# Performance work log

Measured on AMD Instinct MI355X. Metric: run time of the kernel, lower is better.

## Reference

```python
import jax, jax.numpy as jnp
import numpy as np

N = 50000      # nodes
E = 800000     # edges (avg degree 16)
F_IN = 128
HID = 64
NCLS = 40
K = 2          # num_stacks
T = 2          # num_layers (shared weights)


def setup_inputs() -> dict:
    key = jax.random.key(0)
    ks = jax.random.split(key, 10)
    s = 0.05
    return {
        "x": jax.random.normal(ks[0], (N, F_IN), dtype=jnp.float32),
        "edge_index": jax.random.randint(ks[1], (2, E), 0, N),
        "w1_init": jax.random.normal(ks[2], (K, F_IN, HID), dtype=jnp.float32) * s,
        "w1": jax.random.normal(ks[3], (K, HID, HID), dtype=jnp.float32) * s,
        "v1": jax.random.normal(ks[4], (K, F_IN, HID), dtype=jnp.float32) * s,
        "b1": jax.random.normal(ks[5], (K, HID), dtype=jnp.float32) * s,
        "w2_init": jax.random.normal(ks[6], (K, HID, NCLS), dtype=jnp.float32) * s,
        "w2": jax.random.normal(ks[7], (K, NCLS, NCLS), dtype=jnp.float32) * s,
        "v2": jax.random.normal(ks[8], (K, HID, NCLS), dtype=jnp.float32) * s,
        "b2": jax.random.normal(ks[9], (K, NCLS), dtype=jnp.float32) * s,
    }


def _gcn_norm(src, dst, n):
    # PyG gcn_norm with add_self_loops=False: deg over destination, sym norm
    deg = jax.ops.segment_sum(jnp.ones_like(dst, dtype=jnp.float32), dst, num_segments=n)
    dinv = jnp.where(deg > 0, 1.0 / jnp.sqrt(deg), 0.0)
    return dinv[src] * dinv[dst]  # [E]


def _arma_conv(x, src, dst, norm, n, w_init, w, v, b, act):
    # x: [N, Fin]; w_init: [K, Fin, Fout]; w: [K, Fout, Fout]; v: [K, Fin, Fout]; b: [K, Fout]
    root = jnp.einsum('nf,kfg->kng', x, v)  # [K, N, Fout], dropout=0 -> identity
    out = None
    for t in range(T):
        if t == 0:
            h = jnp.einsum('nf,kfg->kng', x, w_init)
        else:
            h = jnp.einsum('knf,kfg->kng', out, w)
        # sparse neighbor aggregation: out[i] = sum_{(j->i)} norm_e * h[j]
        agg = jax.vmap(
            lambda hk: jax.ops.segment_sum(hk[src] * norm[:, None], dst, num_segments=n)
        )(h)  # [K, N, Fout]
        out = act(agg + root + b[:, None, :])
    return out.mean(axis=0)  # mean over stacks -> [N, Fout]


def reference(x, edge_index, w1_init, w1, v1, b1, w2_init, w2, v2, b2):
    src, dst = edge_index[0], edge_index[1]
    norm = _gcn_norm(src, dst, N)
    h = _arma_conv(x, src, dst, norm, N, w1_init, w1, v1, b1, jax.nn.relu)
    h = jax.nn.relu(h)  # wrapper ReLU; dropout is identity in eval
    o = _arma_conv(h, src, dst, norm, N, w2_init, w2, v2, b2, lambda z: z)
    return jax.nn.log_softmax(o, axis=1)
```

## Files before the change

### kernel.cpp

```cpp
#include <hip/hip_runtime.h>
#include <hip/hip_bf16.h>
#include <math.h>

#define N_NODES 50000
#define F_IN 128
#define HID 64
#define NCLS 40
#define K_STACKS 2
#define SCAN_TILE 1024
#define NBLK_CNT 256

typedef __attribute__((ext_vector_type(8))) short short8;
typedef __attribute__((ext_vector_type(4))) float floatx4;
typedef __attribute__((ext_vector_type(2))) float floatx2;

__device__ __forceinline__ unsigned int f32_to_bf16_bits(float f) {
    unsigned int u = __float_as_uint(f);
    return (u + 0x7fffu + ((u >> 16) & 1u)) >> 16;
}
__device__ __forceinline__ unsigned int pack_bf16x2(float a, float b) {
    return f32_to_bf16_bits(a) | (f32_to_bf16_bits(b) << 16);
}
__device__ __forceinline__ unsigned char f32_to_fp8(float v) {
    int pk = __builtin_amdgcn_cvt_pk_fp8_f32(v, v, 0, false);
    return (unsigned char)(pk & 0xff);
}


__global__ __launch_bounds__(256) void count_kernel(const int* __restrict__ dst,
                                                    int* __restrict__ counts,
                                                    int* __restrict__ tileSums, int E) {
    __shared__ int hist[256];
    __shared__ int ts[64];
    int blk = blockIdx.x, t = threadIdx.x;
    hist[t] = 0;
    if (t < 64) ts[t] = 0;
    __syncthreads();
    int chunk = (E + NBLK_CNT - 1) / NBLK_CNT;
    int s = blk * chunk, e = min(E, s + chunk);
    for (int i = s + t; i < e; i += 256) atomicAdd(&hist[dst[i] >> 8], 1);
    __syncthreads();
    counts[t * NBLK_CNT + blk] = hist[t];
    atomicAdd(&ts[t >> 2], hist[t]);
    __syncthreads();
    if (t < 64) atomicAdd(&tileSums[t], ts[t]);
}

__global__ __launch_bounds__(256) void scan_phase3_excl(const int* __restrict__ in,
                                                        const int* __restrict__ tileSums,
                                                        int* __restrict__ out, int n) {
    __shared__ int lds[256];
    __shared__ int tsum[64];
    int b = blockIdx.x, t = threadIdx.x;
    if (t < 64) tsum[t] = tileSums[t];
    int base = b * SCAN_TILE + t * 4;
    int e[4];
    int s = 0;
#pragma unroll
    for (int i = 0; i < 4; ++i) {
        e[i] = (base + i < n) ? in[base + i] : 0;
        s += e[i];
    }
    lds[t] = s;
    __syncthreads();
    int v = s;
    for (int off = 1; off < 256; off <<= 1) {
        int add = (t >= off) ? lds[t - off] : 0;
        __syncthreads();
        v += add;
        lds[t] = v;
        __syncthreads();
    }
    int toff = 0;
    for (int i = 0; i < b; ++i) toff += tsum[i];
    int run = (t == 0 ? 0 : lds[t - 1]) + toff;
#pragma unroll
    for (int i = 0; i < 4; ++i) {
        if (base + i < n) {
            out[base + i] = run;
            run += e[i];
        }
    }
}

__global__ __launch_bounds__(256) void bucket_scatter_kernel(const int* __restrict__ src,
                                                             const int* __restrict__ dst,
                                                             const int* __restrict__ scanned,
                                                             unsigned int* __restrict__ pairs,
                                                             int E) {
    __shared__ int cur[256];
    int blk = blockIdx.x, t = threadIdx.x;
    cur[t] = scanned[t * NBLK_CNT + blk];
    __syncthreads();
    int chunk = (E + NBLK_CNT - 1) / NBLK_CNT;
    int s0 = blk * chunk, e0 = min(E, s0 + chunk);
    for (int i = s0 + t; i < e0; i += 256) {
        int d = dst[i];
        int pos = atomicAdd(&cur[d >> 8], 1);
        pairs[pos] = (unsigned int)src[i] | ((unsigned int)(d & 255) << 16);
    }
}

__global__ __launch_bounds__(256) void csr_build_kernel(const unsigned int* __restrict__ pairs,
                                                        const int* __restrict__ scanned,
                                                        int* __restrict__ row_ptr,
                                                        float* __restrict__ dinv,
                                                        int* __restrict__ col, int N, int E) {
    __shared__ int degl[256], lds[256], curl[256], sb[2];
    int b = blockIdx.x, t = threadIdx.x;
    if (t == 0) {
        sb[0] = scanned[b * NBLK_CNT];
        sb[1] = (b + 1 < 256) ? scanned[(b + 1) * NBLK_CNT] : E;
    }
    degl[t] = 0;
    __syncthreads();
    int bstart = sb[0], bend = sb[1];
    for (int e = bstart + t; e < bend; e += 256) {
        atomicAdd(&degl[(pairs[e] >> 16) & 255], 1);
    }
    __syncthreads();
    int d = degl[t];
    lds[t] = d;
    __syncthreads();
    int v = d;
    for (int off = 1; off < 256; off <<= 1) {
        int add = (t >= off) ? lds[t - off] : 0;
        __syncthreads();
        v += add;
        lds[t] = v;
        __syncthreads();
    }
    int excl = v - d;
    int node = b * 256 + t;
    if (node <= N) row_ptr[node] = bstart + excl;
    if (node < N) dinv[node] = (d > 0) ? (1.0f / sqrtf((float)d)) : 0.0f;
    curl[t] = excl;
    __syncthreads();
    for (int e = bstart + t; e < bend; e += 256) {
        unsigned int p = pairs[e];
        int ln = (p >> 16) & 255;
        int pos = atomicAdd(&curl[ln], 1);
        col[bstart + pos] = (int)(p & 0xffffu);
    }
}

__device__ __forceinline__ void wt_one(const float* __restrict__ in,
                                       unsigned short* __restrict__ out, int li, int C, int F,
                                       int CP) {
    int k = li / (F * CP);
    int r = li - k * F * CP;
    int f = r / CP;
    int c = r - f * CP;
    out[li] = (c < C) ? (unsigned short)f32_to_bf16_bits(in[((size_t)k * C + c) * F + f]) : 0;
}

__global__ void wt_all_kernel(const float* v1, const float* w1i, const float* w1,
                              const float* v2, const float* w2i, const float* w2,
                              unsigned short* v1t, unsigned short* w1it, unsigned short* w1t,
                              unsigned short* v2t, unsigned short* w2it, unsigned short* w2t) {
    int i = blockIdx.x * blockDim.x + threadIdx.x;
    if (i < 16384) wt_one(v1, v1t, i, 128, 64, 128);
    else if (i < 32768) wt_one(w1i, w1it, i - 16384, 128, 64, 128);
    else if (i < 40960) wt_one(w1, w1t, i - 32768, 64, 64, 64);
    else if (i < 46080) wt_one(v2, v2t, i - 40960, 64, 40, 64);
    else if (i < 51200) wt_one(w2i, w2it, i - 46080, 64, 40, 64);
    else if (i < 56320) wt_one(w2, w2t, i - 51200, 40, 40, 64);
}

template <int CINP>
__device__ __forceinline__ void stage_A(const void* A, unsigned short* At, size_t abase,
                                        int n0, int t, int N, int CREAL, int a_bf16) {
    constexpr int CP8 = CINP / 8;
    constexpr int MS = CP8 - 1;
    constexpr int SH = (CP8 == 16) ? 4 : 3;
    for (int i = t; i < 64 * CP8; i += 256) {
        int n = i >> SH;
        int c = i & MS;
        uint4 w = make_uint4(0u, 0u, 0u, 0u);
        int gn = n0 + n;
        if (gn < N && c * 8 < CREAL) {
            if (a_bf16) {
                w = *(const uint4*)((const unsigned short*)A + abase + (size_t)gn * CREAL + c * 8);
            } else {
                const float* srcp = (const float*)A + abase + (size_t)gn * CREAL + c * 8;
                float4 f0 = *(const float4*)(srcp);
                float4 f1 = *(const float4*)(srcp + 4);
                w.x = pack_bf16x2(f0.x, f0.y);
                w.y = pack_bf16x2(f0.z, f0.w);
                w.z = pack_bf16x2(f1.x, f1.y);
                w.w = pack_bf16x2(f1.z, f1.w);
            }
        }
        *(uint4*)(At + n * CINP + ((c ^ (n & MS)) << 3)) = w;
    }
}

template <int CINP>
__device__ __forceinline__ void stage_B(const unsigned short* Bk, unsigned short* Bs, int t,
                                        int COUT) {
    constexpr int CP8 = CINP / 8;
    constexpr int MS = CP8 - 1;
    constexpr int SH = (CP8 == 16) ? 4 : 3;
    for (int i = t; i < COUT * CP8; i += 256) {
        int f = i >> SH;
        int c = i & MS;
        uint4 w = *(const uint4*)(Bk + f * CINP + c * 8);
        *(uint4*)(Bs + f * CINP + ((c ^ (f & MS)) << 3)) = w;
    }
}

__global__ __launch_bounds__(256) void gemm12_kernel(
    const float* __restrict__ A, const unsigned short* __restrict__ Bt1,
    const unsigned short* __restrict__ Bt2, unsigned short* __restrict__ out1,
    unsigned char* __restrict__ out2, const float* __restrict__ scale, int N) {
    constexpr int CINP = 128;
    constexpr int MS = 15;
    __shared__ __align__(16) unsigned short At[64 * CINP];
    __shared__ __align__(16) unsigned short Bs1[64 * CINP];
    __shared__ __align__(16) unsigned short Bs2[64 * CINP];
    const int n0 = blockIdx.x * 64;
    const int t = threadIdx.x;
    stage_A<CINP>(A, At, 0, n0, t, N, CINP, 0);
    const int lane = t & 63;
    const int wv = t >> 6;
    const int quad = lane >> 4;
    const int li = lane & 15;
    const int m0 = wv * 16;
    const int am = (m0 + li) & MS;
#pragma unroll 1
    for (int k = 0; k < 2; ++k) {
        stage_B<CINP>(Bt1 + (size_t)k * 64 * CINP, Bs1, t, 64);
        stage_B<CINP>(Bt2 + (size_t)k * 64 * CINP, Bs2, t, 64);
        __syncthreads();
        floatx4 acc1[4] = {{0.f, 0.f, 0.f, 0.f}, {0.f, 0.f, 0.f, 0.f},
                           {0.f, 0.f, 0.f, 0.f}, {0.f, 0.f, 0.f, 0.f}};
        floatx4 acc2[4] = {{0.f, 0.f, 0.f, 0.f}, {0.f, 0.f, 0.f, 0.f},
                           {0.f, 0.f, 0.f, 0.f}, {0.f, 0.f, 0.f, 0.f}};
#pragma unroll
        for (int kc = 0; kc < 4; ++kc) {
            int cc = kc * 4 + quad;
            short8 a = *(const short8*)(At + (m0 + li) * CINP + ((cc ^ am) << 3));
#pragma unroll
            for (int nt = 0; nt < 4; ++nt) {
                int f = nt * 16 + li;
                int bo = f * CINP + ((cc ^ (f & MS)) << 3);
                short8 b1 = *(const short8*)(Bs1 + bo);
                short8 b2 = *(const short8*)(Bs2 + bo);
                acc1[nt] = __builtin_amdgcn_mfma_f32_16x16x32_bf16(a, b1, acc1[nt], 0, 0, 0);
                acc2[nt] = __builtin_amdgcn_mfma_f32_16x16x32_bf16(a, b2, acc2[nt], 0, 0, 0);
            }
        }
        float sc[4];
#pragma unroll
        for (int r = 0; r < 4; ++r) {
            int node = n0 + m0 + quad * 4 + r;
            sc[r] = (node < N) ? scale[node] : 1.f;
        }
#pragma unroll
        for (int nt = 0; nt < 4; ++nt) {
            int f = nt * 16 + li;
#pragma unroll
            for (int r = 0; r < 4; ++r) {
                int node = n0 + m0 + quad * 4 + r;
                if (node < N) {
                    out1[((size_t)k * N + node) * 64 + f] =
                        (unsigned short)f32_to_bf16_bits(acc1[nt][r]);
                    out2[(size_t)node * 128 + (size_t)k * 64 + f] = f32_to_fp8(acc2[nt][r] * sc[r]);
                }
            }
        }
        __syncthreads();
    }
}

template <int F, int COUT, int FMODE>
__global__ __launch_bounds__(256) void agg_gemm_kernel(
    const unsigned char* __restrict__ h8, const int* __restrict__ row_ptr,
    const int* __restrict__ col, const float* __restrict__ dinv,
    const unsigned short* __restrict__ rootb, const float* __restrict__ bias,
    const unsigned short* __restrict__ Bt1, const unsigned short* __restrict__ Bt2,
    unsigned short* __restrict__ rootOut, unsigned char* __restrict__ tblOut, int N) {
    constexpr int NA = (FMODE == 1) ? 1 : 2;
    constexpr int NB = (FMODE == 1) ? 4 : 2;
    constexpr int BT = COUT * 64;
    constexpr int NT = (COUT + 15) / 16;
    constexpr int FH = F / 8;
    constexpr int ROWB = 2 * F;
    __shared__ __align__(16) unsigned short At[NA * 64 * 64];
    __shared__ __align__(16) unsigned short Bs[NB * BT];
    __shared__ int rp[65];
    __shared__ float dvl[64];

    const int n0 = blockIdx.x * 64;
    const int t = threadIdx.x;

    stage_B<64>(Bt1, Bs, t, COUT);
    stage_B<64>(Bt1 + (size_t)COUT * 64, Bs + BT, t, COUT);
    if constexpr (FMODE == 1) {
        stage_B<64>(Bt2, Bs + 2 * BT, t, COUT);
        stage_B<64>(Bt2 + (size_t)COUT * 64, Bs + 3 * BT, t, COUT);
    }
    if (t < 65) rp[t] = row_ptr[min(n0 + t, N)];
    if (t < 64) dvl[t] = (n0 + t < N) ? dinv[n0 + t] : 0.f;
    __syncthreads();

    const int lane = t & 63;
    const int wv = t >> 6;
    const int half = lane >> 5;
    const int l32 = lane & 31;
    const int sub = l32 >> 4;
    const int fq = l32 & 15;
    const int kk = fq >> 3;
    const int fqq = fq & 7;
    const int fqc = (fqq < FH) ? fqq : (FH - 1);
    const int foff = kk * F + fqc * 8;

#pragma unroll 1
    for (int p = 0; p < 8; ++p) {
        const int nl = wv * 16 + p * 2 + half;
        const int node = n0 + nl;
        const bool valid = node < N;
        const int e0 = rp[nl];
        const int deg = rp[nl + 1] - e0;
        const float dv = dvl[nl];
        float acc[8] = {};
        for (int w0 = 0; w0 < deg; w0 += 32) {
            int mye = w0 + l32;
            int c = (mye < deg) ? col[e0 + mye] : 0;
            int nch = min(deg - w0, 32);
            for (int base = 0; base < nch; base += 16) {
                uint2 v[8];
                float wj[8];
#pragma unroll
                for (int u = 0; u < 8; ++u) {
                    int j = base + u * 2 + sub;
                    int cj = __shfl(c, (half << 5) | (j & 31));
                    bool ok = (j < nch);
                    wj[u] = ok ? 1.f : 0.f;
                    int cs = ok ? cj : 0;
                    v[u] = *(const uint2*)(h8 + (size_t)cs * ROWB + foff);
                }
#pragma unroll
                for (int u = 0; u < 8; ++u) {
                    floatx2 f0 = __builtin_amdgcn_cvt_pk_f32_fp8(v[u].x, false);
                    floatx2 f1 = __builtin_amdgcn_cvt_pk_f32_fp8(v[u].x, true);
                    floatx2 f2 = __builtin_amdgcn_cvt_pk_f32_fp8(v[u].y, false);
                    floatx2 f3 = __builtin_amdgcn_cvt_pk_f32_fp8(v[u].y, true);
                    acc[0] += wj[u] * f0.x;
                    acc[1] += wj[u] * f0.y;
                    acc[2] += wj[u] * f1.x;
                    acc[3] += wj[u] * f1.y;
                    acc[4] += wj[u] * f2.x;
                    acc[5] += wj[u] * f2.y;
                    acc[6] += wj[u] * f3.x;
                    acc[7] += wj[u] * f3.y;
                }
            }
        }
#pragma unroll
        for (int i = 0; i < 8; ++i) acc[i] += __shfl_xor(acc[i], 16);

        size_t oc = ((size_t)kk * N + (valid ? node : 0)) * F + fqc * 8;
        uint4 rv = *(const uint4*)(rootb + oc);
        const float* bp = bias + kk * F + fqc * 8;
        float4 b0 = *(const float4*)(bp);
        float4 b1_ = *(const float4*)(bp + 4);
        const unsigned int ru[4] = {rv.x, rv.y, rv.z, rv.w};
        float res[8];
#pragma unroll
        for (int q = 0; q < 4; ++q) {
            float rlo = __uint_as_float(ru[q] << 16);
            float rhi = __uint_as_float(ru[q] & 0xffff0000u);
            float blo = (q < 2) ? ((q == 0) ? b0.x : b0.z) : ((q == 2) ? b1_.x : b1_.z);
            float bhi = (q < 2) ? ((q == 0) ? b0.y : b0.w) : ((q == 2) ? b1_.y : b1_.w);
            res[2 * q] = acc[2 * q] * dv + rlo + blo;
            res[2 * q + 1] = acc[2 * q + 1] * dv + rhi + bhi;
        }
        if constexpr (FMODE != 2) {
#pragma unroll
            for (int i = 0; i < 8; ++i) res[i] = fmaxf(res[i], 0.f);
        }
        if constexpr (FMODE == 1) {
            float mres[8];
#pragma unroll
            for (int i = 0; i < 8; ++i) mres[i] = 0.5f * (res[i] + __shfl_xor(res[i], 8));
            if (sub == 0 && kk == 0) {
                uint4 w;
                w.x = pack_bf16x2(mres[0], mres[1]);
                w.y = pack_bf16x2(mres[2], mres[3]);
                w.z = pack_bf16x2(mres[4], mres[5]);
                w.w = pack_bf16x2(mres[6], mres[7]);
                *(uint4*)(At + nl * 64 + ((fqq ^ (nl & 7)) << 3)) = w;
            }
        } else {
            if (sub == 0) {
                uint4 w = make_uint4(0u, 0u, 0u, 0u);
                if (fqq < FH) {
                    w.x = pack_bf16x2(res[0], res[1]);
                    w.y = pack_bf16x2(res[2], res[3]);
                    w.z = pack_bf16x2(res[4], res[5]);
                    w.w = pack_bf16x2(res[6], res[7]);
                }
                *(uint4*)(At + kk * 4096 + nl * 64 + ((fqq ^ (nl & 7)) << 3)) = w;
            }
        }
    }
    __syncthreads();

    const int quad = lane >> 4;
    const int li = lane & 15;
    const int m0 = wv * 16;
    const int am = (m0 + li) & 7;

    if constexpr (FMODE == 1) {
        floatx4 aR[2][NT] = {};
        floatx4 aT[2][NT] = {};
#pragma unroll
        for (int kc = 0; kc < 2; ++kc) {
            int cc = kc * 4 + quad;
            short8 a = *(const short8*)(At + (m0 + li) * 64 + ((cc ^ am) << 3));
#pragma unroll
            for (int nt = 0; nt < NT; ++nt) {
                int f = nt * 16 + li;
                int fc = (COUT & 15) ? ((f < COUT) ? f : (COUT - 1)) : f;
                int bo = fc * 64 + ((cc ^ (fc & 7)) << 3);
#pragma unroll
                for (int k = 0; k < 2; ++k) {
                    short8 bR = *(const short8*)(Bs + k * BT + bo);
                    short8 bT = *(const short8*)(Bs + (2 + k) * BT + bo);
                    aR[k][nt] = __builtin_amdgcn_mfma_f32_16x16x32_bf16(a, bR, aR[k][nt], 0, 0, 0);
                    aT[k][nt] = __builtin_amdgcn_mfma_f32_16x16x32_bf16(a, bT, aT[k][nt], 0, 0, 0);
                }
            }
        }
#pragma unroll
        for (int k = 0; k < 2; ++k) {
#pragma unroll
            for (int nt = 0; nt < NT; ++nt) {
                int f = nt * 16 + li;
                if (f >= COUT) continue;
#pragma unroll
                for (int r = 0; r < 4; ++r) {
                    int nl2 = m0 + quad * 4 + r;
                    int node = n0 + nl2;
                    if (node < N) {
                        rootOut[((size_t)k * N + node) * COUT + f] =
                            (unsigned short)f32_to_bf16_bits(aR[k][nt][r]);
                        tblOut[(size_t)node * 2 * COUT + (size_t)k * COUT + f] =
                            f32_to_fp8(aT[k][nt][r] * dvl[nl2]);
                    }
                }
            }
        }
    } else {
        floatx4 ac[2][NT] = {};
#pragma unroll
        for (int kc = 0; kc < 2; ++kc) {
            int cc = kc * 4 + quad;
            int ao = (m0 + li) * 64 + ((cc ^ am) << 3);
            short8 a0 = *(const short8*)(At + ao);
            short8 a1 = *(const short8*)(At + 4096 + ao);
#pragma unroll
            for (int nt = 0; nt < NT; ++nt) {
                int f = nt * 16 + li;
                int fc = (COUT & 15) ? ((f < COUT) ? f : (COUT - 1)) : f;
                int bo = fc * 64 + ((cc ^ (fc & 7)) << 3);
                short8 b0 = *(const short8*)(Bs + bo);
                short8 b1v = *(const short8*)(Bs + BT + bo);
                ac[0][nt] = __builtin_amdgcn_mfma_f32_16x16x32_bf16(a0, b0, ac[0][nt], 0, 0, 0);
                ac[1][nt] = __builtin_amdgcn_mfma_f32_16x16x32_bf16(a1, b1v, ac[1][nt], 0, 0, 0);
            }
        }
#pragma unroll
        for (int k = 0; k < 2; ++k) {
#pragma unroll
            for (int nt = 0; nt < NT; ++nt) {
                int f = nt * 16 + li;
                if (f >= COUT) continue;
#pragma unroll
                for (int r = 0; r < 4; ++r) {
                    int nl2 = m0 + quad * 4 + r;
                    int node = n0 + nl2;
                    if (node < N)
                        tblOut[(size_t)node * 2 * COUT + (size_t)k * COUT + f] =
                            f32_to_fp8(ac[k][nt][r] * dvl[nl2]);
                }
            }
        }
    }
}

template <int F>
__global__ __launch_bounds__(256) void agg_kernel(
    const unsigned char* __restrict__ h8, const int* __restrict__ row_ptr,
    const int* __restrict__ col, const float* __restrict__ dinv,
    const unsigned short* __restrict__ rootb, const float* __restrict__ bias,
    void* __restrict__ out, int N, int do_relu, int mode) {
    constexpr int FH = F / 8;
    constexpr int ROWB = 2 * F;
    int wid = (blockIdx.x * blockDim.x + threadIdx.x) >> 6;
    int lane = threadIdx.x & 63;
    int half = lane >> 5;
    int l32 = lane & 31;
    int node = wid * 2 + half;
    bool valid = node < N;
    int e0 = 0, deg = 0;
    float dv = 0.f;
    if (valid) {
        e0 = row_ptr[node];
        deg = row_ptr[node + 1] - e0;
        dv = dinv[node];
    }
    const int sub = l32 >> 4;
    const int fq = l32 & 15;
    const int kk = fq >> 3;
    const int fqq = fq & 7;
    const int fqc = (fqq < FH) ? fqq : (FH - 1);
    const int foff = kk * F + fqc * 8;

    float acc[8] = {};
    for (int w0 = 0; w0 < deg; w0 += 32) {
        int mye = w0 + l32;
        int c = (mye < deg) ? col[e0 + mye] : 0;
        int nch = min(deg - w0, 32);
        for (int base = 0; base < nch; base += 16) {
            uint2 v[8];
            float wj[8];
#pragma unroll
            for (int u = 0; u < 8; ++u) {
                int j = base + u * 2 + sub;
                int cj = __shfl(c, (half << 5) | (j & 31));
                bool ok = (j < nch);
                wj[u] = ok ? 1.f : 0.f;
                int cs = ok ? cj : 0;
                v[u] = *(const uint2*)(h8 + (size_t)cs * ROWB + foff);
            }
#pragma unroll
            for (int u = 0; u < 8; ++u) {
                floatx2 f0 = __builtin_amdgcn_cvt_pk_f32_fp8(v[u].x, false);
                floatx2 f1 = __builtin_amdgcn_cvt_pk_f32_fp8(v[u].x, true);
                floatx2 f2 = __builtin_amdgcn_cvt_pk_f32_fp8(v[u].y, false);
                floatx2 f3 = __builtin_amdgcn_cvt_pk_f32_fp8(v[u].y, true);
                acc[0] += wj[u] * f0.x;
                acc[1] += wj[u] * f0.y;
                acc[2] += wj[u] * f1.x;
                acc[3] += wj[u] * f1.y;
                acc[4] += wj[u] * f2.x;
                acc[5] += wj[u] * f2.y;
                acc[6] += wj[u] * f3.x;
                acc[7] += wj[u] * f3.y;
            }
        }
    }
#pragma unroll
    for (int i = 0; i < 8; ++i) acc[i] += __shfl_xor(acc[i], 16);

    size_t oc = ((size_t)kk * N + (valid ? node : 0)) * F + fqc * 8;
    uint4 rv = *(const uint4*)(rootb + oc);
    const float* bp = bias + kk * F + fqc * 8;
    float4 b0 = *(const float4*)(bp);
    float4 b1 = *(const float4*)(bp + 4);
    const unsigned int ru[4] = {rv.x, rv.y, rv.z, rv.w};
    float res[8];
#pragma unroll
    for (int q = 0; q < 4; ++q) {
        float rlo = __uint_as_float(ru[q] << 16);
        float rhi = __uint_as_float(ru[q] & 0xffff0000u);
        float blo = (q < 2) ? ((q == 0) ? b0.x : b0.z) : ((q == 2) ? b1.x : b1.z);
        float bhi = (q < 2) ? ((q == 0) ? b0.y : b0.w) : ((q == 2) ? b1.y : b1.w);
        res[2 * q] = acc[2 * q] * dv + rlo + blo;
        res[2 * q + 1] = acc[2 * q + 1] * dv + rhi + bhi;
    }
    if (do_relu) {
#pragma unroll
        for (int i = 0; i < 8; ++i) res[i] = fmaxf(res[i], 0.f);
    }
    if (mode == 0) {
        if (sub == 0 && fqq < FH && valid) {
            size_t o = ((size_t)kk * N + node) * F + fqq * 8;
            uint4 w;
            w.x = pack_bf16x2(res[0], res[1]);
            w.y = pack_bf16x2(res[2], res[3]);
            w.z = pack_bf16x2(res[4], res[5]);
            w.w = pack_bf16x2(res[6], res[7]);
            *(uint4*)((unsigned short*)out + o) = w;
        }
    } else {
        float mres[8];
#pragma unroll
        for (int i = 0; i < 8; ++i) mres[i] = 0.5f * (res[i] + __shfl_xor(res[i], 8));
        if (mode == 1) {
            if (sub == 0 && kk == 0 && fqq < FH && valid) {
                size_t o = (size_t)node * F + fqq * 8;
                *(float4*)((float*)out + o) = make_float4(mres[0], mres[1], mres[2], mres[3]);
                *(float4*)((float*)out + o + 4) = make_float4(mres[4], mres[5], mres[6], mres[7]);
            }
        } else {
            bool act = (fqq < FH);
            float lm = -INFINITY;
            if (act) {
#pragma unroll
                for (int i = 0; i < 8; ++i) lm = fmaxf(lm, mres[i]);
            }
#pragma unroll
            for (int m = 1; m < 8; m <<= 1) lm = fmaxf(lm, __shfl_xor(lm, m));
            float ls = 0.f;
            if (act) {
#pragma unroll
                for (int i = 0; i < 8; ++i) ls += expf(mres[i] - lm);
            }
#pragma unroll
            for (int m = 1; m < 8; m <<= 1) ls += __shfl_xor(ls, m);
            float lg = lm + logf(ls);
            if (sub == 0 && kk == 0 && act && valid) {
                size_t o = (size_t)node * F + fqq * 8;
                *(float4*)((float*)out + o) =
                    make_float4(mres[0] - lg, mres[1] - lg, mres[2] - lg, mres[3] - lg);
                *(float4*)((float*)out + o + 4) =
                    make_float4(mres[4] - lg, mres[5] - lg, mres[6] - lg, mres[7] - lg);
            }
        }
    }
}


static inline size_t align256(size_t x) { return (x + 255) & ~(size_t)255; }

extern "C" void kernel_launch(void* const* d_in, const int* in_sizes, int n_in,
                              void* d_out, int out_size, void* d_ws, size_t ws_size,
                              hipStream_t stream) {
    const float* x = (const float*)d_in[0];
    const int* ei = (const int*)d_in[1];
    const float* w1_init = (const float*)d_in[2];
    const float* w1 = (const float*)d_in[3];
    const float* v1 = (const float*)d_in[4];
    const float* b1 = (const float*)d_in[5];
    const float* w2_init = (const float*)d_in[6];
    const float* w2 = (const float*)d_in[7];
    const float* v2 = (const float*)d_in[8];
    const float* b2 = (const float*)d_in[9];

    const int N = in_sizes[0] / F_IN;
    const int E = in_sizes[1] / 2;
    const int* src = ei;
    const int* dst = ei + E;

    char* p = (char*)d_ws;
    auto take = [&](size_t bytes) {
        char* r = p;
        p += align256(bytes);
        return r;
    };
    float* dinv = (float*)take((size_t)N * 4);
    int* row_ptr = (int*)take((size_t)(N + 1) * 4);
    int* tileSums = (int*)take(256 * 4);
    int* counts = (int*)take((size_t)256 * NBLK_CNT * 4);
    int* scanned = (int*)take((size_t)256 * NBLK_CNT * 4);
    unsigned int* pairs = (unsigned int*)take((size_t)E * 4);
    int* col = (int*)take((size_t)E * 4);
    unsigned short* v1t = (unsigned short*)take((size_t)2 * 64 * 128 * 2);
    unsigned short* w1it = (unsigned short*)take((size_t)2 * 64 * 128 * 2);
    unsigned short* w1t = (unsigned short*)take((size_t)2 * 64 * 64 * 2);
    unsigned short* v2t = (unsigned short*)take((size_t)2 * 40 * 64 * 2);
    unsigned short* w2it = (unsigned short*)take((size_t)2 * 40 * 64 * 2);
    unsigned short* w2t = (unsigned short*)take((size_t)2 * 40 * 64 * 2);
    unsigned short* rootb = (unsigned short*)take((size_t)K_STACKS * N * HID * 2);
    unsigned short* root2 = (unsigned short*)take((size_t)K_STACKS * N * NCLS * 2);
    unsigned char* tblA = (unsigned char*)take((size_t)K_STACKS * N * HID);
    unsigned char* tblB = (unsigned char*)take((size_t)K_STACKS * N * HID);

    const int TB = 256;
    const int nCnt = 256 * NBLK_CNT;
    const int nScanBlocks = nCnt / SCAN_TILE;
    const int nBuckets = (N + 255) / 256;
    const int ntiles = (N + 63) / 64;

    hipMemsetAsync(tileSums, 0, 256, stream);
    count_kernel<<<NBLK_CNT, 256, 0, stream>>>(dst, counts, tileSums, E);
    scan_phase3_excl<<<nScanBlocks, 256, 0, stream>>>(counts, tileSums, scanned, nCnt);
    bucket_scatter_kernel<<<NBLK_CNT, 256, 0, stream>>>(src, dst, scanned, pairs, E);
    csr_build_kernel<<<nBuckets, 256, 0, stream>>>(pairs, scanned, row_ptr, dinv, col, N, E);

    wt_all_kernel<<<(56320 + TB - 1) / TB, TB, 0, stream>>>(v1, w1_init, w1, v2, w2_init, w2,
                                                            v1t, w1it, w1t, v2t, w2it, w2t);

    const int agg_blocks = ((N + 1) / 2 + 3) / 4;

    gemm12_kernel<<<ntiles, 256, 0, stream>>>(x, v1t, w1it, rootb, tblA, dinv, N);
    agg_gemm_kernel<HID, HID, 0><<<ntiles, 256, 0, stream>>>(
        tblA, row_ptr, col, dinv, rootb, b1, w1t, nullptr, nullptr, tblB, N);

    agg_gemm_kernel<HID, NCLS, 1><<<ntiles, 256, 0, stream>>>(
        tblB, row_ptr, col, dinv, rootb, b1, v2t, w2it, root2, tblA, N);

    agg_gemm_kernel<NCLS, NCLS, 2><<<ntiles, 256, 0, stream>>>(
        tblA, row_ptr, col, dinv, root2, b2, w2t, nullptr, nullptr, tblB, N);

    agg_kernel<NCLS><<<agg_blocks, 256, 0, stream>>>(tblB, row_ptr, col, dinv, root2, b2,
                                                     (float*)d_out, N, 0, 2);
}
```

Measured before the change: 302.3 us.

## Split stacks across grid and waves; use 512-thread fused agg-gemm blocks

The first dense GEMM kernel is generalized and launched on a 2D grid, one block per (tile, stack), instead of looping over both stacks inside each block. The fused aggregation+GEMM kernels move to 512-thread blocks, so each wave aggregates half as many nodes and in the MFMA phase each wave handles a single stack (kSel). The aim is more parallelism and shorter per-wave serial work. The cost is that each GEMM block restages the A tile, and the larger blocks carry more register and LDS pressure that may reduce occupancy.

```diff
diff --git a/kernel.cpp b/kernel.cpp
--- a/kernel.cpp
+++ b/kernel.cpp
@@ -169,11 +169,12 @@
 
 template <int CINP>
 __device__ __forceinline__ void stage_A(const void* A, unsigned short* At, size_t abase,
-                                        int n0, int t, int N, int CREAL, int a_bf16) {
+                                        int n0, int t, int N, int CREAL, int a_bf16,
+                                        int stride) {
     constexpr int CP8 = CINP / 8;
     constexpr int MS = CP8 - 1;
     constexpr int SH = (CP8 == 16) ? 4 : 3;
-    for (int i = t; i < 64 * CP8; i += 256) {
+    for (int i = t; i < 64 * CP8; i += stride) {
         int n = i >> SH;
         int c = i & MS;
         uint4 w = make_uint4(0u, 0u, 0u, 0u);
@@ -197,11 +198,11 @@
 
 template <int CINP>
 __device__ __forceinline__ void stage_B(const unsigned short* Bk, unsigned short* Bs, int t,
-                                        int COUT) {
+                                        int COUT, int stride) {
     constexpr int CP8 = CINP / 8;
     constexpr int MS = CP8 - 1;
     constexpr int SH = (CP8 == 16) ? 4 : 3;
-    for (int i = t; i < COUT * CP8; i += 256) {
+    for (int i = t; i < COUT * CP8; i += stride) {
         int f = i >> SH;
         int c = i & MS;
         uint4 w = *(const uint4*)(Bk + f * CINP + c * 8);
@@ -209,39 +210,43 @@
     }
 }
 
-__global__ __launch_bounds__(256) void gemm12_kernel(
-    const float* __restrict__ A, const unsigned short* __restrict__ Bt1,
+template <int CINP>
+__global__ __launch_bounds__(256) void gemm2_mfma(
+    const void* __restrict__ A, const unsigned short* __restrict__ Bt1,
     const unsigned short* __restrict__ Bt2, unsigned short* __restrict__ out1,
-    unsigned char* __restrict__ out2, const float* __restrict__ scale, int N) {
-    constexpr int CINP = 128;
-    constexpr int MS = 15;
+    unsigned char* __restrict__ out2, const float* __restrict__ scale, int N, int COUT,
+    int CREAL, int a_bf16) {
+    constexpr int MS = CINP / 8 - 1;
     __shared__ __align__(16) unsigned short At[64 * CINP];
     __shared__ __align__(16) unsigned short Bs1[64 * CINP];
     __shared__ __align__(16) unsigned short Bs2[64 * CINP];
+
+    const int k = blockIdx.y;
     const int n0 = blockIdx.x * 64;
     const int t = threadIdx.x;
-    stage_A<CINP>(A, At, 0, n0, t, N, CINP, 0);
+    stage_A<CINP>(A, At, (size_t)0, n0, t, N, CREAL, a_bf16, 256);
+    stage_B<CINP>(Bt1 + (size_t)k * COUT * CINP, Bs1, t, COUT, 256);
+    stage_B<CINP>(Bt2 + (size_t)k * COUT * CINP, Bs2, t, COUT, 256);
+    __syncthreads();
+
     const int lane = t & 63;
     const int wv = t >> 6;
     const int quad = lane >> 4;
     const int li = lane & 15;
     const int m0 = wv * 16;
+
+    floatx4 acc1[4] = {{0.f, 0.f, 0.f, 0.f}, {0.f, 0.f, 0.f, 0.f},
+                       {0.f, 0.f, 0.f, 0.f}, {0.f, 0.f, 0.f, 0.f}};
+    floatx4 acc2[4] = {{0.f, 0.f, 0.f, 0.f}, {0.f, 0.f, 0.f, 0.f},
+                       {0.f, 0.f, 0.f, 0.f}, {0.f, 0.f, 0.f, 0.f}};
     const int am = (m0 + li) & MS;
-#pragma unroll 1
-    for (int k = 0; k < 2; ++k) {
-        stage_B<CINP>(Bt1 + (size_t)k * 64 * CINP, Bs1, t, 64);
-        stage_B<CINP>(Bt2 + (size_t)k * 64 * CINP, Bs2, t, 64);
-        __syncthreads();
-        floatx4 acc1[4] = {{0.f, 0.f, 0.f, 0.f}, {0.f, 0.f, 0.f, 0.f},
-                           {0.f, 0.f, 0.f, 0.f}, {0.f, 0.f, 0.f, 0.f}};
-        floatx4 acc2[4] = {{0.f, 0.f, 0.f, 0.f}, {0.f, 0.f, 0.f, 0.f},
-                           {0.f, 0.f, 0.f, 0.f}, {0.f, 0.f, 0.f, 0.f}};
-#pragma unroll
-        for (int kc = 0; kc < 4; ++kc) {
-            int cc = kc * 4 + quad;
-            short8 a = *(const short8*)(At + (m0 + li) * CINP + ((cc ^ am) << 3));
-#pragma unroll
-            for (int nt = 0; nt < 4; ++nt) {
+#pragma unroll
+    for (int kc = 0; kc < CINP / 32; ++kc) {
+        int cc = kc * 4 + quad;
+        short8 a = *(const short8*)(At + (m0 + li) * CINP + ((cc ^ am) << 3));
+#pragma unroll
+        for (int nt = 0; nt < 4; ++nt) {
+            if (nt * 16 < COUT) {
                 int f = nt * 16 + li;
                 int bo = f * CINP + ((cc ^ (f & MS)) << 3);
                 short8 b1 = *(const short8*)(Bs1 + bo);
@@ -250,31 +255,34 @@
                 acc2[nt] = __builtin_amdgcn_mfma_f32_16x16x32_bf16(a, b2, acc2[nt], 0, 0, 0);
             }
         }
-        float sc[4];
+    }
+
+    float sc[4];
+#pragma unroll
+    for (int r = 0; r < 4; ++r) {
+        int node = n0 + m0 + quad * 4 + r;
+        sc[r] = (node < N) ? scale[node] : 1.f;
+    }
+#pragma unroll
+    for (int nt = 0; nt < 4; ++nt) {
+        if (nt * 16 >= COUT) continue;
+        int f = nt * 16 + li;
+        if (f >= COUT) continue;
 #pragma unroll
         for (int r = 0; r < 4; ++r) {
             int node = n0 + m0 + quad * 4 + r;
-            sc[r] = (node < N) ? scale[node] : 1.f;
-        }
-#pragma unroll
-        for (int nt = 0; nt < 4; ++nt) {
-            int f = nt * 16 + li;
-#pragma unroll
-            for (int r = 0; r < 4; ++r) {
-                int node = n0 + m0 + quad * 4 + r;
-                if (node < N) {
-                    out1[((size_t)k * N + node) * 64 + f] =
-                        (unsigned short)f32_to_bf16_bits(acc1[nt][r]);
-                    out2[(size_t)node * 128 + (size_t)k * 64 + f] = f32_to_fp8(acc2[nt][r] * sc[r]);
-                }
-            }
-        }
-        __syncthreads();
+            if (node < N) {
+                out1[((size_t)k * N + node) * COUT + f] =
+                    (unsigned short)f32_to_bf16_bits(acc1[nt][r]);
+                out2[(size_t)node * 2 * COUT + (size_t)k * COUT + f] =
+                    f32_to_fp8(acc2[nt][r] * sc[r]);
+            }
+        }
     }
 }
 
 template <int F, int COUT, int FMODE>
-__global__ __launch_bounds__(256) void agg_gemm_kernel(
+__global__ __launch_bounds__(512) void agg_gemm_kernel(
     const unsigned char* __restrict__ h8, const int* __restrict__ row_ptr,
     const int* __restrict__ col, const float* __restrict__ dinv,
     const unsigned short* __restrict__ rootb, const float* __restrict__ bias,
@@ -294,11 +302,11 @@
     const int n0 = blockIdx.x * 64;
     const int t = threadIdx.x;
 
-    stage_B<64>(Bt1, Bs, t, COUT);
-    stage_B<64>(Bt1 + (size_t)COUT * 64, Bs + BT, t, COUT);
+    stage_B<64>(Bt1, Bs, t, COUT, 512);
+    stage_B<64>(Bt1 + (size_t)COUT * 64, Bs + BT, t, COUT, 512);
     if constexpr (FMODE == 1) {
-        stage_B<64>(Bt2, Bs + 2 * BT, t, COUT);
-        stage_B<64>(Bt2 + (size_t)COUT * 64, Bs + 3 * BT, t, COUT);
+        stage_B<64>(Bt2, Bs + 2 * BT, t, COUT, 512);
+        stage_B<64>(Bt2 + (size_t)COUT * 64, Bs + 3 * BT, t, COUT, 512);
     }
     if (t < 65) rp[t] = row_ptr[min(n0 + t, N)];
     if (t < 64) dvl[t] = (n0 + t < N) ? dinv[n0 + t] : 0.f;
@@ -316,8 +324,8 @@
     const int foff = kk * F + fqc * 8;
 
 #pragma unroll 1
-    for (int p = 0; p < 8; ++p) {
-        const int nl = wv * 16 + p * 2 + half;
+    for (int p = 0; p < 4; ++p) {
+        const int nl = wv * 8 + p * 2 + half;
         const int node = n0 + nl;
         const bool valid = node < N;
         const int e0 = rp[nl];
@@ -409,12 +417,13 @@
 
     const int quad = lane >> 4;
     const int li = lane & 15;
-    const int m0 = wv * 16;
+    const int kSel = wv >> 2;
+    const int m0 = (wv & 3) * 16;
     const int am = (m0 + li) & 7;
 
     if constexpr (FMODE == 1) {
-        floatx4 aR[2][NT] = {};
-        floatx4 aT[2][NT] = {};
+        floatx4 aR[NT] = {};
+        floatx4 aT[NT] = {};
 #pragma unroll
         for (int kc = 0; kc < 2; ++kc) {
             int cc = kc * 4 + quad;
@@ -424,67 +433,54 @@
                 int f = nt * 16 + li;
                 int fc = (COUT & 15) ? ((f < COUT) ? f : (COUT - 1)) : f;
                 int bo = fc * 64 + ((cc ^ (fc & 7)) << 3);
-#pragma unroll
-                for (int k = 0; k < 2; ++k) {
-                    short8 bR = *(const short8*)(Bs + k * BT + bo);
-                    short8 bT = *(const short8*)(Bs + (2 + k) * BT + bo);
-                    aR[k][nt] = __builtin_amdgcn_mfma_f32_16x16x32_bf16(a, bR, aR[k][nt], 0, 0, 0);
-                    aT[k][nt] = __builtin_amdgcn_mfma_f32_16x16x32_bf16(a, bT, aT[k][nt], 0, 0, 0);
+                short8 bR = *(const short8*)(Bs + kSel * BT + bo);
+                short8 bT = *(const short8*)(Bs + (2 + kSel) * BT + bo);
+                aR[nt] = __builtin_amdgcn_mfma_f32_16x16x32_bf16(a, bR, aR[nt], 0, 0, 0);
+                aT[nt] = __builtin_amdgcn_mfma_f32_16x16x32_bf16(a, bT, aT[nt], 0, 0, 0);
+            }
+        }
+#pragma unroll
+        for (int nt = 0; nt < NT; ++nt) {
+            int f = nt * 16 + li;
+            if (f >= COUT) continue;
+#pragma unroll
+            for (int r = 0; r < 4; ++r) {
+                int nl2 = m0 + quad * 4 + r;
+                int node = n0 + nl2;
+                if (node < N) {
+                    rootOut[((size_t)kSel * N + node) * COUT + f] =
+                        (unsigned short)f32_to_bf16_bits(aR[nt][r]);
+                    tblOut[(size_t)node * 2 * COUT + (size_t)kSel * COUT + f] =
+                        f32_to_fp8(aT[nt][r] * dvl[nl2]);
                 }
             }
         }
-#pragma unroll
-        for (int k = 0; k < 2; ++k) {
-#pragma unroll
-            for (int nt = 0; nt < NT; ++nt) {
-                int f = nt * 16 + li;
-                if (f >= COUT) continue;
-#pragma unroll
-                for (int r = 0; r < 4; ++r) {
-                    int nl2 = m0 + quad * 4 + r;
-                    int node = n0 + nl2;
-                    if (node < N) {
-                        rootOut[((size_t)k * N + node) * COUT + f] =
-                            (unsigned short)f32_to_bf16_bits(aR[k][nt][r]);
-                        tblOut[(size_t)node * 2 * COUT + (size_t)k * COUT + f] =
-                            f32_to_fp8(aT[k][nt][r] * dvl[nl2]);
-                    }
-                }
-            }
-        }
     } else {
-        floatx4 ac[2][NT] = {};
+        floatx4 ac[NT] = {};
 #pragma unroll
         for (int kc = 0; kc < 2; ++kc) {
             int cc = kc * 4 + quad;
-            int ao = (m0 + li) * 64 + ((cc ^ am) << 3);
-            short8 a0 = *(const short8*)(At + ao);
-            short8 a1 = *(const short8*)(At + 4096 + ao);
+            short8 a = *(const short8*)(At + kSel * 4096 + (m0 + li) * 64 + ((cc ^ am) << 3));
 #pragma unroll
             for (int nt = 0; nt < NT; ++nt) {
                 int f = nt * 16 + li;
                 int fc = (COUT & 15) ? ((f < COUT) ? f : (COUT - 1)) : f;
                 int bo = fc * 64 + ((cc ^ (fc & 7)) << 3);
-                short8 b0 = *(const short8*)(Bs + bo);
-                short8 b1v = *(const short8*)(Bs + BT + bo);
-                ac[0][nt] = __builtin_amdgcn_mfma_f32_16x16x32_bf16(a0, b0, ac[0][nt], 0, 0, 0);
-                ac[1][nt] = __builtin_amdgcn_mfma_f32_16x16x32_bf16(a1, b1v, ac[1][nt], 0, 0, 0);
-            }
-        }
-#pragma unroll
-        for (int k = 0; k < 2; ++k) {
-#pragma unroll
-            for (int nt = 0; nt < NT; ++nt) {
-                int f = nt * 16 + li;
-                if (f >= COUT) continue;
-#pragma unroll
-                for (int r = 0; r < 4; ++r) {
-                    int nl2 = m0 + quad * 4 + r;
-                    int node = n0 + nl2;
-                    if (node < N)
-                        tblOut[(size_t)node * 2 * COUT + (size_t)k * COUT + f] =
-                            f32_to_fp8(ac[k][nt][r] * dvl[nl2]);
-                }
+                short8 b = *(const short8*)(Bs + kSel * BT + bo);
+                ac[nt] = __builtin_amdgcn_mfma_f32_16x16x32_bf16(a, b, ac[nt], 0, 0, 0);
+            }
+        }
+#pragma unroll
+        for (int nt = 0; nt < NT; ++nt) {
+            int f = nt * 16 + li;
+            if (f >= COUT) continue;
+#pragma unroll
+            for (int r = 0; r < 4; ++r) {
+                int nl2 = m0 + quad * 4 + r;
+                int node = n0 + nl2;
+                if (node < N)
+                    tblOut[(size_t)node * 2 * COUT + (size_t)kSel * COUT + f] =
+                        f32_to_fp8(ac[nt][r] * dvl[nl2]);
             }
         }
     }
@@ -684,16 +680,17 @@
     wt_all_kernel<<<(56320 + TB - 1) / TB, TB, 0, stream>>>(v1, w1_init, w1, v2, w2_init, w2,
                                                             v1t, w1it, w1t, v2t, w2it, w2t);
 
+    dim3 ggrid(ntiles, K_STACKS);
     const int agg_blocks = ((N + 1) / 2 + 3) / 4;
 
-    gemm12_kernel<<<ntiles, 256, 0, stream>>>(x, v1t, w1it, rootb, tblA, dinv, N);
-    agg_gemm_kernel<HID, HID, 0><<<ntiles, 256, 0, stream>>>(
+    gemm2_mfma<128><<<ggrid, 256, 0, stream>>>(x, v1t, w1it, rootb, tblA, dinv, N, HID, 128, 0);
+    agg_gemm_kernel<HID, HID, 0><<<ntiles, 512, 0, stream>>>(
         tblA, row_ptr, col, dinv, rootb, b1, w1t, nullptr, nullptr, tblB, N);
 
-    agg_gemm_kernel<HID, NCLS, 1><<<ntiles, 256, 0, stream>>>(
+    agg_gemm_kernel<HID, NCLS, 1><<<ntiles, 512, 0, stream>>>(
         tblB, row_ptr, col, dinv, rootb, b1, v2t, w2it, root2, tblA, N);
 
-    agg_gemm_kernel<NCLS, NCLS, 2><<<ntiles, 256, 0, stream>>>(
+    agg_gemm_kernel<NCLS, NCLS, 2><<<ntiles, 512, 0, stream>>>(
         tblA, row_ptr, col, dinv, root2, b2, w2t, nullptr, nullptr, tblB, N);
 
     agg_kernel<NCLS><<<agg_blocks, 256, 0, stream>>>(tblB, row_ptr, col, dinv, root2, b2,
```

Result: faster. 274.4 us (-9.2%).
